# Kernel tuning notes

Hardware: AMD Instinct MI355X
Metric: run time of the kernel (lower is better)

The kernel has to match this reference:

```python
import jax, jax.numpy as jnp
import numpy as np

# ---- init_kwargs-derived constants ----
B, IN_F, OUT_F = 8192, 4096, 4096
W_SCALE = 0.01          # layer_params['w_scale']
B_SCALE = 0.01          # layer_params['b_scale']
IN_MIN, IN_MAX = -1.0, 1.0   # input_stats
NUM_BITS = 8
QMAX = 2 ** NUM_BITS - 1
IN_SCALE = (IN_MAX - IN_MIN) / QMAX
IN_ZP = int(round(-IN_MIN / (IN_SCALE + 1e-12)))


def setup_inputs() -> dict:
    key = jax.random.key(0)
    k1, k2, k3 = jax.random.split(key, 3)
    x_float = jax.random.normal(k1, (B, IN_F), dtype=jnp.float32)
    # int8-range weights/bias (stored as int32 containers)
    w_q = jax.random.randint(k2, (OUT_F, IN_F), -128, 128, dtype=jnp.int32)
    b_q = jax.random.randint(k3, (OUT_F,), -128, 128, dtype=jnp.int32)
    return {"x_float": x_float, "w_q": w_q, "b_q": b_q}


def reference(x_float, w_q, b_q):
    # quantize input to uint8 range [0,255]
    x_q = jnp.clip(jnp.round(x_float / IN_SCALE + IN_ZP), 0, 255).astype(jnp.int32)
    x_shifted = x_q - IN_ZP                       # [B, IN_F] int32
    # exact int32 accumulation matmul: [B, IN_F] @ [IN_F, OUT_F]
    acc_int = jnp.matmul(x_shifted, w_q.T, preferred_element_type=jnp.int32)
    out = acc_int.astype(jnp.float32) * (IN_SCALE * W_SCALE)
    out = out + b_q.astype(jnp.float32) * B_SCALE  # bias_float = b_q * b_scale
    return out
```

## Files before the change

### kernel.cpp

```cpp
#include <hip/hip_runtime.h>
#include <stdint.h>

constexpr int Mdim = 8192;
constexpr int Ndim = 4096;
constexpr int Kdim = 4096;
constexpr int NSTEP = Kdim / 64;

#define ISF        ((float)(2.0 / 255.0))
#define OUT_SCALE  ((float)(2.0 / 255.0 * 0.01))
#define BSCALE     0.01f

typedef int i32x4 __attribute__((ext_vector_type(4)));

__global__ __launch_bounds__(256) void quantize_x(const float* __restrict__ x,
                                                  int* __restrict__ x8,
                                                  int ngroups) {
  int idx = blockIdx.x * 256 + threadIdx.x;
  int stride = gridDim.x * 256;
  for (int g = idx; g < ngroups; g += stride) {
    float4 v = reinterpret_cast<const float4*>(x)[g];
    int a0 = (int)rintf(v.x / ISF + 127.0f);
    int a1 = (int)rintf(v.y / ISF + 127.0f);
    int a2 = (int)rintf(v.z / ISF + 127.0f);
    int a3 = (int)rintf(v.w / ISF + 127.0f);
    a0 = a0 < 0 ? 0 : (a0 > 255 ? 255 : a0); a0 -= 128;
    a1 = a1 < 0 ? 0 : (a1 > 255 ? 255 : a1); a1 -= 128;
    a2 = a2 < 0 ? 0 : (a2 > 255 ? 255 : a2); a2 -= 128;
    a3 = a3 < 0 ? 0 : (a3 > 255 ? 255 : a3); a3 -= 128;
    x8[g] = (a0 & 0xff) | ((a1 & 0xff) << 8) | ((a2 & 0xff) << 16) |
            (int)(((unsigned)(a3 & 0xff)) << 24);
  }
}

__global__ __launch_bounds__(256) void convert_w(const int* __restrict__ wq,
                                                 int* __restrict__ w8,
                                                 int* __restrict__ wsum) {
  int row = blockIdx.x;
  const int4* src = reinterpret_cast<const int4*>(wq + (size_t)row * Kdim);
  int* dst = w8 + (size_t)row * (Kdim / 4);
  int s = 0;
#pragma unroll
  for (int i = 0; i < 4; ++i) {
    int idx = i * 256 + threadIdx.x;
    int4 v = src[idx];
    s += v.x + v.y + v.z + v.w;
    dst[idx] = (v.x & 0xff) | ((v.y & 0xff) << 8) | ((v.z & 0xff) << 16) |
               (int)(((unsigned)(v.w & 0xff)) << 24);
  }
  __shared__ int red[256];
  red[threadIdx.x] = s;
  __syncthreads();
  for (int off = 128; off; off >>= 1) {
    if ((int)threadIdx.x < off) red[threadIdx.x] += red[threadIdx.x + off];
    __syncthreads();
  }
  if (threadIdx.x == 0) wsum[row] = red[0];
}

#define AS1C const __attribute__((address_space(1))) void*
#define AS3  __attribute__((address_space(3))) void*
#define GLL(src, dst) __builtin_amdgcn_global_load_lds((AS1C)(src), (AS3)(dst), 16, 0, 0)
#define BAR() asm volatile("s_barrier" ::: "memory")
#define VMC(N) asm volatile("s_waitcnt vmcnt(" #N ")" ::: "memory")
#define MFMA(a, b, c) __builtin_amdgcn_mfma_i32_16x16x64_i8(a, b, c, 0, 0, 0)

__global__ __launch_bounds__(256, 2) void gemm_i8_db(const int8_t* __restrict__ A8,
                                                     const int8_t* __restrict__ B8,
                                                     const int* __restrict__ wsum,
                                                     const int* __restrict__ bq,
                                                     float* __restrict__ out) {
  __shared__ uint8_t lds[65536];

  int bid = blockIdx.x;
  int wg = (bid & 7) * 128 + (bid >> 3);
  int bm = wg >> 5;
  int bn = wg & 31;

  const int tid = threadIdx.x;
  const int lane = tid & 63;
  const int wv = tid >> 6;
  const int wr = wv >> 1;
  const int wc = wv & 1;
  const int l15 = lane & 15, hi = lane >> 4;

  size_t aSrc[4];
  int aDstB[4];
#pragma unroll
  for (int is = 0; is < 4; ++is) {
    int e = is * 256 + tid;
    int r = e >> 2, s = e & 3;
    aSrc[is] = (size_t)(bm * 256 + r) * Kdim + ((s ^ (r & 3)) << 4);
    aDstB[is] = is * 4096 + wv * 1024;
  }
  size_t bSrc[2];
  int bDstB[2];
#pragma unroll
  for (int is = 0; is < 2; ++is) {
    int e = is * 256 + tid;
    int r = e >> 2, s = e & 3;
    bSrc[is] = (size_t)(bn * 128 + r) * Kdim + ((s ^ (r & 3)) << 4);
    bDstB[is] = is * 4096 + wv * 1024;
  }

#define ISSUE_A(P, t) do { \
    _Pragma("unroll") for (int is = 0; is < 4; ++is) \
      GLL(A8 + aSrc[is] + (size_t)(t) * 64, &lds[(P) * 16384 + aDstB[is]]); \
  } while (0)
#define ISSUE_B(P, t) do { \
    _Pragma("unroll") for (int is = 0; is < 2; ++is) \
      GLL(B8 + bSrc[is] + (size_t)(t) * 64, &lds[49152 + (P) * 8192 + bDstB[is]]); \
  } while (0)

  const int sl = (hi ^ (l15 & 3)) << 4;
  const int aFrag = (wr * 128 + l15) * 64 + sl;
  const int bFrag = (wc * 64 + l15) * 64 + sl;

#define LDA(P, i) (*reinterpret_cast<const i32x4*>(&lds[(P) * 16384 + aFrag + (i) * 1024]))
#define LDB(P, j) (*reinterpret_cast<const i32x4*>(&lds[49152 + (P) * 8192 + bFrag + (j) * 1024]))

  i32x4 acc[8][4];
#pragma unroll
  for (int i = 0; i < 8; ++i)
#pragma unroll
    for (int j = 0; j < 4; ++j) acc[i][j] = (i32x4){0, 0, 0, 0};

  ISSUE_A(0, 0);
  ISSUE_B(0, 0);
  ISSUE_A(1, 1);
  VMC(4);
  BAR();

#define STEP(PA, PB, PB1, PA2, t, DOB, DOA, VM4, VM0) do { \
    if (DOB) ISSUE_B(PB1, (t) + 1); \
    if (DOA) ISSUE_A(PA2, (t) + 2); \
    i32x4 a_[8], b_[4]; \
    _Pragma("unroll") for (int j = 0; j < 4; ++j) b_[j] = LDB(PB, j); \
    _Pragma("unroll") for (int i = 0; i < 8; ++i) a_[i] = LDA(PA, i); \
    __builtin_amdgcn_s_setprio(1); \
    _Pragma("unroll") for (int i = 0; i < 8; ++i) \
      _Pragma("unroll") for (int j = 0; j < 4; ++j) \
        acc[i][j] = MFMA(a_[i], b_[j], acc[i][j]); \
    __builtin_amdgcn_s_setprio(0); \
    if (VM4) VMC(4); \
    if (VM0) VMC(0); \
    BAR(); \
  } while (0)

  for (int it = 0; it < 10; ++it) {
    int t = it * 6;
    STEP(0, 0, 1, 2, t + 0, 1, 1, 1, 0);
    STEP(1, 1, 0, 0, t + 1, 1, 1, 1, 0);
    STEP(2, 0, 1, 1, t + 2, 1, 1, 1, 0);
    STEP(0, 1, 0, 2, t + 3, 1, 1, 1, 0);
    STEP(1, 0, 1, 0, t + 4, 1, 1, 1, 0);
    STEP(2, 1, 0, 1, t + 5, 1, 1, 1, 0);
  }
  STEP(0, 0, 1, 2, 60, 1, 1, 1, 0);
  STEP(1, 1, 0, 0, 61, 1, 1, 1, 0);
  STEP(2, 0, 1, 0, 62, 1, 0, 0, 1);
  STEP(0, 1, 0, 0, 63, 0, 0, 0, 0);

#pragma unroll
  for (int j = 0; j < 4; ++j) {
    int col = bn * 128 + wc * 64 + j * 16 + l15;
    float fb = (float)bq[col] * BSCALE;
    int ws = wsum[col];
#pragma unroll
    for (int i = 0; i < 8; ++i) {
      int rbase = bm * 256 + wr * 128 + i * 16 + hi * 4;
#pragma unroll
      for (int p = 0; p < 4; ++p)
        out[(size_t)(rbase + p) * Ndim + col] = (float)(acc[i][j][p] + ws) * OUT_SCALE + fb;
    }
  }
#undef STEP
#undef ISSUE_A
#undef ISSUE_B
#undef LDA
#undef LDB
}

__global__ void fallback_kernel(const float* __restrict__ x, const int* __restrict__ wq,
                                const int* __restrict__ bq, float* __restrict__ out) {
  int col = blockIdx.x * 16 + (threadIdx.x & 15);
  int row = blockIdx.y * 16 + (threadIdx.x >> 4);
  const float* xr = x + (size_t)row * Kdim;
  const int* wr_ = wq + (size_t)col * Kdim;
  int acc = 0;
  for (int k = 0; k < Kdim; ++k) {
    int v = (int)rintf(xr[k] / ISF + 127.0f);
    v = v < 0 ? 0 : (v > 255 ? 255 : v);
    acc += (v - 127) * wr_[k];
  }
  out[(size_t)row * Ndim + col] = (float)acc * OUT_SCALE + (float)bq[col] * BSCALE;
}

extern "C" void kernel_launch(void* const* d_in, const int* in_sizes, int n_in,
                              void* d_out, int out_size, void* d_ws, size_t ws_size,
                              hipStream_t stream) {
  const float* x = (const float*)d_in[0];
  const int* wq = (const int*)d_in[1];
  const int* bq = (const int*)d_in[2];
  float* out = (float*)d_out;

  const size_t x8_bytes = (size_t)Mdim * Kdim;
  const size_t w8_bytes = (size_t)Ndim * Kdim;
  const size_t ws_need = x8_bytes + w8_bytes + (size_t)Ndim * sizeof(int);

  if (ws_size >= ws_need) {
    int8_t* x8 = (int8_t*)d_ws;
    int8_t* w8 = x8 + x8_bytes;
    int* wsum = (int*)(w8 + w8_bytes);

    quantize_x<<<2048, 256, 0, stream>>>(x, (int*)x8, Mdim * Kdim / 4);
    convert_w<<<Ndim, 256, 0, stream>>>(wq, (int*)w8, wsum);
    gemm_i8_db<<<(Mdim / 256) * (Ndim / 128), 256, 0, stream>>>(x8, w8, wsum, bq, out);
  } else {
    dim3 grid(Ndim / 16, Mdim / 16);
    fallback_kernel<<<grid, 256, 0, stream>>>(x, wq, bq, out);
  }
}
```

Before: 203.5 us.

## Restructure int8 GEMM into 8-wave blocks with K=128 tiles and interleaved fragment loads

The int8 MFMA GEMM now runs 512-thread blocks (8 waves, each owning a 64x64 sub-tile) and uses a K step of 128 with triple-buffered A/B tiles, about 144KB of LDS per block. Each tile is split into two K-halves, and LDS fragment loads are interleaved between MFMA groups in a software-pipelined ping-pong, with global prefetch issued mid-tile. The aim is to halve the number of barriers per K, hide LDS latency behind MFMAs and overlap global loads better. The large LDS footprint limits the CU to one block, so occupancy now depends on intra-block scheduling, and the LDS swizzle is widened to 8 slots.

```diff
diff --git a/kernel.cpp b/kernel.cpp
--- a/kernel.cpp
+++ b/kernel.cpp
@@ -4,7 +4,7 @@
 constexpr int Mdim = 8192;
 constexpr int Ndim = 4096;
 constexpr int Kdim = 4096;
-constexpr int NSTEP = Kdim / 64;
+constexpr int NT = Kdim / 128;
 
 #define ISF        ((float)(2.0 / 255.0))
 #define OUT_SCALE  ((float)(2.0 / 255.0 * 0.01))
@@ -64,12 +64,12 @@
 #define VMC(N) asm volatile("s_waitcnt vmcnt(" #N ")" ::: "memory")
 #define MFMA(a, b, c) __builtin_amdgcn_mfma_i32_16x16x64_i8(a, b, c, 0, 0, 0)
 
-__global__ __launch_bounds__(256, 2) void gemm_i8_db(const int8_t* __restrict__ A8,
+__global__ __launch_bounds__(512, 2) void gemm_i8_pw(const int8_t* __restrict__ A8,
                                                      const int8_t* __restrict__ B8,
                                                      const int* __restrict__ wsum,
                                                      const int* __restrict__ bq,
                                                      float* __restrict__ out) {
-  __shared__ uint8_t lds[65536];
+  __shared__ uint8_t lds[147456];
 
   int bid = blockIdx.x;
   int wg = (bid & 7) * 128 + (bid >> 3);
@@ -84,81 +84,105 @@
   const int l15 = lane & 15, hi = lane >> 4;
 
   size_t aSrc[4];
-  int aDstB[4];
 #pragma unroll
   for (int is = 0; is < 4; ++is) {
-    int e = is * 256 + tid;
-    int r = e >> 2, s = e & 3;
-    aSrc[is] = (size_t)(bm * 256 + r) * Kdim + ((s ^ (r & 3)) << 4);
-    aDstB[is] = is * 4096 + wv * 1024;
+    int e = is * 512 + tid;
+    int r = e >> 3, s = e & 7;
+    aSrc[is] = (size_t)(bm * 256 + r) * Kdim + ((s ^ (r & 7)) << 4);
   }
   size_t bSrc[2];
-  int bDstB[2];
 #pragma unroll
   for (int is = 0; is < 2; ++is) {
-    int e = is * 256 + tid;
-    int r = e >> 2, s = e & 3;
-    bSrc[is] = (size_t)(bn * 128 + r) * Kdim + ((s ^ (r & 3)) << 4);
-    bDstB[is] = is * 4096 + wv * 1024;
-  }
+    int e = is * 512 + tid;
+    int r = e >> 3, s = e & 7;
+    bSrc[is] = (size_t)(bn * 128 + r) * Kdim + ((s ^ (r & 7)) << 4);
+  }
+  const int ldsw = wv * 1024;
 
 #define ISSUE_A(P, t) do { \
     _Pragma("unroll") for (int is = 0; is < 4; ++is) \
-      GLL(A8 + aSrc[is] + (size_t)(t) * 64, &lds[(P) * 16384 + aDstB[is]]); \
+      GLL(A8 + aSrc[is] + (size_t)(t) * 128, &lds[(P) * 32768 + is * 8192 + ldsw]); \
   } while (0)
 #define ISSUE_B(P, t) do { \
     _Pragma("unroll") for (int is = 0; is < 2; ++is) \
-      GLL(B8 + bSrc[is] + (size_t)(t) * 64, &lds[49152 + (P) * 8192 + bDstB[is]]); \
+      GLL(B8 + bSrc[is] + (size_t)(t) * 128, &lds[98304 + (P) * 16384 + is * 8192 + ldsw]); \
   } while (0)
 
-  const int sl = (hi ^ (l15 & 3)) << 4;
-  const int aFrag = (wr * 128 + l15) * 64 + sl;
-  const int bFrag = (wc * 64 + l15) * 64 + sl;
-
-#define LDA(P, i) (*reinterpret_cast<const i32x4*>(&lds[(P) * 16384 + aFrag + (i) * 1024]))
-#define LDB(P, j) (*reinterpret_cast<const i32x4*>(&lds[49152 + (P) * 8192 + bFrag + (j) * 1024]))
-
-  i32x4 acc[8][4];
-#pragma unroll
-  for (int i = 0; i < 8; ++i)
+  const int aRow = (wr * 64 + l15) * 128;
+  const int bRow = (wc * 64 + l15) * 128;
+  const int sl0 = (hi ^ (l15 & 7)) << 4;
+  const int sl1 = ((4 + hi) ^ (l15 & 7)) << 4;
+
+#define LDA(P, i, ks) (*reinterpret_cast<const i32x4*>( \
+    &lds[(P) * 32768 + aRow + (i) * 2048 + ((ks) ? sl1 : sl0)]))
+#define LDB(P, j, ks) (*reinterpret_cast<const i32x4*>( \
+    &lds[98304 + (P) * 16384 + bRow + (j) * 2048 + ((ks) ? sl1 : sl0)]))
+
+  i32x4 acc[4][4];
+#pragma unroll
+  for (int i = 0; i < 4; ++i)
 #pragma unroll
     for (int j = 0; j < 4; ++j) acc[i][j] = (i32x4){0, 0, 0, 0};
 
-  ISSUE_A(0, 0);
-  ISSUE_B(0, 0);
-  ISSUE_A(1, 1);
-  VMC(4);
+  i32x4 a0[4], a1[4], B0[4], B1[4];
+
+  ISSUE_A(0, 0); ISSUE_B(0, 0);
+  ISSUE_A(1, 1); ISSUE_B(1, 1);
+  VMC(6);
   BAR();
-
-#define STEP(PA, PB, PB1, PA2, t, DOB, DOA, VM4, VM0) do { \
-    if (DOB) ISSUE_B(PB1, (t) + 1); \
-    if (DOA) ISSUE_A(PA2, (t) + 2); \
-    i32x4 a_[8], b_[4]; \
-    _Pragma("unroll") for (int j = 0; j < 4; ++j) b_[j] = LDB(PB, j); \
-    _Pragma("unroll") for (int i = 0; i < 8; ++i) a_[i] = LDA(PA, i); \
-    __builtin_amdgcn_s_setprio(1); \
-    _Pragma("unroll") for (int i = 0; i < 8; ++i) \
-      _Pragma("unroll") for (int j = 0; j < 4; ++j) \
-        acc[i][j] = MFMA(a_[i], b_[j], acc[i][j]); \
-    __builtin_amdgcn_s_setprio(0); \
-    if (VM4) VMC(4); \
+#pragma unroll
+  for (int i = 0; i < 4; ++i) a0[i] = LDA(0, i, 0);
+  B0[0] = LDB(0, 0, 0); B0[1] = LDB(0, 1, 0);
+
+#define TILE(TB, TN, TG, t, DOG, VM6, VM0, CROSS, DOBAR) do { \
+     \
+    B0[2] = LDB(TB, 2, 0); B0[3] = LDB(TB, 3, 0); \
+    B1[0] = LDB(TB, 0, 1); B1[1] = LDB(TB, 1, 1); \
+    __builtin_amdgcn_s_setprio(1); \
+    _Pragma("unroll") for (int i = 0; i < 4; ++i) { \
+      acc[i][0] = MFMA(a0[i], B0[0], acc[i][0]); \
+      acc[i][1] = MFMA(a0[i], B0[1], acc[i][1]); } \
+    __builtin_amdgcn_s_setprio(0); \
+     \
+    _Pragma("unroll") for (int i = 0; i < 4; ++i) a1[i] = LDA(TB, i, 1); \
+    B1[2] = LDB(TB, 2, 1); B1[3] = LDB(TB, 3, 1); \
+    __builtin_amdgcn_s_setprio(1); \
+    _Pragma("unroll") for (int i = 0; i < 4; ++i) { \
+      acc[i][2] = MFMA(a0[i], B0[2], acc[i][2]); \
+      acc[i][3] = MFMA(a0[i], B0[3], acc[i][3]); } \
+    __builtin_amdgcn_s_setprio(0); \
+     \
+    if (DOG) { ISSUE_A(TG, (t) + 2); ISSUE_B(TG, (t) + 2); } \
+    __builtin_amdgcn_s_setprio(1); \
+    _Pragma("unroll") for (int i = 0; i < 4; ++i) { \
+      acc[i][0] = MFMA(a1[i], B1[0], acc[i][0]); \
+      acc[i][1] = MFMA(a1[i], B1[1], acc[i][1]); } \
+    __builtin_amdgcn_s_setprio(0); \
+    if (VM6) VMC(6); \
     if (VM0) VMC(0); \
-    BAR(); \
+    if (DOBAR) BAR(); \
+     \
+    if (CROSS) { \
+      _Pragma("unroll") for (int i = 0; i < 4; ++i) a0[i] = LDA(TN, i, 0); \
+      B0[0] = LDB(TN, 0, 0); B0[1] = LDB(TN, 1, 0); } \
+    __builtin_amdgcn_s_setprio(1); \
+    _Pragma("unroll") for (int i = 0; i < 4; ++i) { \
+      acc[i][2] = MFMA(a1[i], B1[2], acc[i][2]); \
+      acc[i][3] = MFMA(a1[i], B1[3], acc[i][3]); } \
+    __builtin_amdgcn_s_setprio(0); \
   } while (0)
 
-  for (int it = 0; it < 10; ++it) {
-    int t = it * 6;
-    STEP(0, 0, 1, 2, t + 0, 1, 1, 1, 0);
-    STEP(1, 1, 0, 0, t + 1, 1, 1, 1, 0);
-    STEP(2, 0, 1, 1, t + 2, 1, 1, 1, 0);
-    STEP(0, 1, 0, 2, t + 3, 1, 1, 1, 0);
-    STEP(1, 0, 1, 0, t + 4, 1, 1, 1, 0);
-    STEP(2, 1, 0, 1, t + 5, 1, 1, 1, 0);
-  }
-  STEP(0, 0, 1, 2, 60, 1, 1, 1, 0);
-  STEP(1, 1, 0, 0, 61, 1, 1, 1, 0);
-  STEP(2, 0, 1, 0, 62, 1, 0, 0, 1);
-  STEP(0, 1, 0, 0, 63, 0, 0, 0, 0);
+  for (int it = 0; it < NT / 3 - 1; ++it) {
+    int t = it * 3;
+    TILE(0, 1, 2, t + 0, 1, 1, 0, 1, 1);
+    TILE(1, 2, 0, t + 1, 1, 1, 0, 1, 1);
+    TILE(2, 0, 1, t + 2, 1, 1, 0, 1, 1);
+  }
+  TILE(0, 1, 2, 27, 1, 1, 0, 1, 1);
+  TILE(1, 2, 0, 28, 1, 1, 0, 1, 1);
+  TILE(2, 0, 1, 29, 1, 1, 0, 1, 1);
+  TILE(0, 1, 2, 30, 0, 0, 1, 1, 1);
+  TILE(1, 2, 0, 31, 0, 0, 0, 0, 0);
 
 #pragma unroll
   for (int j = 0; j < 4; ++j) {
@@ -166,14 +190,14 @@
     float fb = (float)bq[col] * BSCALE;
     int ws = wsum[col];
 #pragma unroll
-    for (int i = 0; i < 8; ++i) {
-      int rbase = bm * 256 + wr * 128 + i * 16 + hi * 4;
+    for (int i = 0; i < 4; ++i) {
+      int rbase = bm * 256 + wr * 64 + i * 16 + hi * 4;
 #pragma unroll
       for (int p = 0; p < 4; ++p)
         out[(size_t)(rbase + p) * Ndim + col] = (float)(acc[i][j][p] + ws) * OUT_SCALE + fb;
     }
   }
-#undef STEP
+#undef TILE
 #undef ISSUE_A
 #undef ISSUE_B
 #undef LDA
@@ -214,7 +238,7 @@
 
     quantize_x<<<2048, 256, 0, stream>>>(x, (int*)x8, Mdim * Kdim / 4);
     convert_w<<<Ndim, 256, 0, stream>>>(wq, (int*)w8, wsum);
-    gemm_i8_db<<<(Mdim / 256) * (Ndim / 128), 256, 0, stream>>>(x8, w8, wsum, bq, out);
+    gemm_i8_pw<<<(Mdim / 256) * (Ndim / 128), 512, 0, stream>>>(x8, w8, wsum, bq, out);
   } else {
     dim3 grid(Ndim / 16, Mdim / 16);
     fallback_kernel<<<grid, 256, 0, stream>>>(x, wq, bq, out);
```

Result: faster. 192.0 us (-5.6%).
